# Kernel tuning notes

Hardware: AMD Instinct MI355X
Metric: run time of the kernel (lower is better)

## Reference

```python
import jax, jax.numpy as jnp
import numpy as np

N = 8192          # number of signals (rows of Y)
DIM_BASIS = 512   # signal dimension n
NUM_BASIS = 2048  # dictionary atoms m (overcomplete)
SC_ITERS = 20     # FISTA iterations
PM_ITERS = 100    # power-method iterations


def setup_inputs() -> dict:
    key = jax.random.key(0)
    kY, kW = jax.random.split(key)
    Y = jax.random.normal(kY, (N, DIM_BASIS), jnp.float32)
    W = jax.random.normal(kW, (DIM_BASIS, NUM_BASIS), jnp.float32)
    # NormDict applied in __init__: unit-norm columns
    W = W / jnp.linalg.norm(W, axis=0, keepdims=True)
    K = jnp.asarray(0.1, jnp.float32)  # lamda for FISTA soft-threshold
    return {"Y": Y, "W": W, "K": K}


def _soft(x, lam):
    return jnp.sign(x) * jax.nn.relu(jnp.abs(x) - lam)


def _power_method(W):
    # largest eigenvalue of W^T W (W: [n, m]); fixed random init for determinism
    X0 = jax.random.normal(jax.random.key(1), (1, W.shape[1]), W.dtype)

    def body(i, carry):
        X, _ = carry
        X = (X @ W.T) @ W          # X <- X W^T W, shape [1, m]
        nm = jnp.linalg.norm(X)
        return (X / nm, nm)

    _, nm = jax.lax.fori_loop(0, PM_ITERS, body, (X0, jnp.asarray(1.0, W.dtype)))
    return nm


def _fista(Y, W, lam, iters):
    c = _power_method(W)
    eta = 1.0 / c
    Gamma0 = _soft(Y @ (eta * W), lam)     # [N, m]
    Yn = jnp.linalg.norm(Y)

    def step(carry, _):
        Gamma, Z, t = carry
        residual = Z @ W.T - Y                              # [N, n]
        Gamma_new = _soft(Z - eta * (residual @ W), lam / c)
        t_new = (1.0 + jnp.sqrt(1.0 + 4.0 * t * t)) / 2.0
        Z_new = Gamma_new + ((t - 1.0) / t_new) * (Gamma_new - Gamma)
        nrm = jnp.linalg.norm(residual) / Yn
        return (Gamma_new, Z_new, t_new), nrm

    init = (Gamma0, Gamma0, jnp.asarray(1.0, Y.dtype))
    (Gamma, _, _), norms = jax.lax.scan(step, init, None, length=iters)
    return Gamma, norms


def reference(Y, W, K):
    # NormDict at start of forward (done on .data in torch -> no grad through norm)
    Wn = W / jax.lax.stop_gradient(jnp.linalg.norm(W, axis=0, keepdims=True))
    # W.requires_grad_(False) during sparse coding
    W_ng = jax.lax.stop_gradient(Wn)
    Gamma, norms = _fista(Y, W_ng, K, SC_ITERS)
    X = Gamma @ Wn.T   # reconstruction, grad flows to W here only
    return X, Gamma, norms
```

## Files before the change

### kernel.cpp

```cpp
#include <hip/hip_runtime.h>
#include <cmath>

#define NR   8192
#define DB   512
#define NB   2048
#define ITERS 20
#define NSQ   9

typedef _Float16 hfrag_t __attribute__((ext_vector_type(8)));
typedef __attribute__((ext_vector_type(4))) float accv_t;
typedef unsigned short us4 __attribute__((ext_vector_type(4)));
typedef unsigned short us8 __attribute__((ext_vector_type(8)));
typedef float f4 __attribute__((ext_vector_type(4)));

#define SL_Y2   0
#define SL_NUM  1
#define SL_DEN  2
#define SL_C    3
#define SL_ETA  4
#define SL_THR  5
#define SL_TR   6
#define SL_RES2 16

__device__ inline unsigned short f2h(float f) {
  _Float16 h = (_Float16)f;
  return __builtin_bit_cast(unsigned short, h);
}
__device__ inline float h2f(unsigned short u) {
  _Float16 h = __builtin_bit_cast(_Float16, u);
  return (float)h;
}
__device__ inline float softthr(float x, float t) {
  float a = fabsf(x) - t;
  return a > 0.f ? copysignf(a, x) : 0.f;
}


template<int MI, int NI, int NKT>
__device__ inline void gemm_tt(const unsigned short* __restrict__ At, int NTka,
                               const unsigned short* __restrict__ Bt, int NTkb,
                               int mt0, int nt0, accv_t acc[MI][NI]) {
  const int lane = threadIdx.x & 63;
  const int l16 = lane & 15, quad = lane >> 4;
  const int off = l16 * 16 + (quad & 1) * 8;
  const int kh = quad >> 1;
#pragma unroll
  for (int mi = 0; mi < MI; ++mi)
#pragma unroll
    for (int ni = 0; ni < NI; ++ni) acc[mi][ni] = (accv_t){0.f, 0.f, 0.f, 0.f};

#pragma unroll 4
  for (int kt = 0; kt < NKT; ++kt) {
    const int ktile = (kt << 1) + kh;
    hfrag_t af[MI], bf[NI];
#pragma unroll
    for (int mi = 0; mi < MI; ++mi)
      af[mi] = *(const hfrag_t*)&At[(((size_t)(mt0 + mi) * NTka + ktile) << 8) + off];
#pragma unroll
    for (int ni = 0; ni < NI; ++ni)
      bf[ni] = *(const hfrag_t*)&Bt[(((size_t)(nt0 + ni) * NTkb + ktile) << 8) + off];
#pragma unroll
    for (int mi = 0; mi < MI; ++mi)
#pragma unroll
      for (int ni = 0; ni < NI; ++ni)
        acc[mi][ni] = __builtin_amdgcn_mfma_f32_16x16x32_f16(bf[ni], af[mi], acc[mi][ni], 0, 0, 0);
  }
}

__device__ inline size_t ctile_off(int mt, int nt, int NTn) {
  int lane = threadIdx.x & 63;
  return (((size_t)mt * NTn + nt) << 8) + (lane & 15) * 16 + (lane >> 4) * 4;
}

__global__ void k_zero(float* slots, float* colsq) {
  if (threadIdx.x < 64) slots[threadIdx.x] = 0.f;
  for (int i = threadIdx.x; i < NB; i += 256) colsq[i] = 0.f;
}

__global__ void k_colsq(const float* __restrict__ W, float* __restrict__ colsq) {
  int j = blockIdx.x * 256 + threadIdx.x;
  int r0 = blockIdx.y * 64;
  float s = 0.f;
  for (int i = 0; i < 64; ++i) { float v = W[(size_t)(r0 + i) * NB + j]; s += v * v; }
  atomicAdd(&colsq[j], s);
}

__global__ void k_wnorm(const float* __restrict__ W, const float* __restrict__ colsq,
                        unsigned short* __restrict__ Wn_t, unsigned short* __restrict__ Wt_t) {
  int tx = threadIdx.x & 31, ty = threadIdx.x >> 5;
  int j = blockIdx.x * 32 + tx;
  float inv = 1.0f / sqrtf(colsq[j]);
#pragma unroll
  for (int r = 0; r < 4; ++r) {
    int i = blockIdx.y * 32 + ty + r * 8;
    unsigned short h = f2h(W[(size_t)i * NB + j] * inv);
    Wn_t[(((size_t)(i >> 4) * (NB / 16) + (j >> 4)) << 8) + (i & 15) * 16 + (j & 15)] = h;
    Wt_t[(((size_t)(j >> 4) * (DB / 16) + (i >> 4)) << 8) + (j & 15) * 16 + (i & 15)] = h;
  }
}

__global__ __launch_bounds__(256) void k_ynorm(const float* __restrict__ Y,
                                               unsigned short* __restrict__ Yh,
                                               float* __restrict__ slots) {
  __shared__ float part[4];
  int w = threadIdx.x >> 6, lane = threadIdx.x & 63;
  float s = 0.f;
#pragma unroll
  for (int rr = 0; rr < 4; ++rr) {
    int m = blockIdx.x * 16 + w * 4 + rr;
    const float* yrow = &Y[(size_t)m * DB + lane * 8];
    f4 v0 = *(const f4*)yrow;
    f4 v1 = *(const f4*)(yrow + 4);
    us8 h;
#pragma unroll
    for (int q = 0; q < 4; ++q) {
      h[q] = f2h(v0[q]);     s += v0[q] * v0[q];
      h[4 + q] = f2h(v1[q]); s += v1[q] * v1[q];
    }
    *(us8*)&Yh[(((size_t)(m >> 4) * 32 + (lane >> 1)) << 8) + (m & 15) * 16 + (lane & 1) * 8] = h;
  }
  for (int off = 32; off > 0; off >>= 1) s += __shfl_xor(s, off);
  if (lane == 0) part[w] = s;
  __syncthreads();
  if (threadIdx.x == 0) atomicAdd(&slots[SL_Y2], part[0] + part[1] + part[2] + part[3]);
}

__global__ __launch_bounds__(256) void k_sq(const float* __restrict__ S, float* __restrict__ D,
                                            const float* __restrict__ trIn, float* __restrict__ trOut) {
  __shared__ float tA[32][33], tB[32][33];
  int tx = threadIdx.x & 31, ty = threadIdx.x >> 5;
  int r0 = blockIdx.y * 32, c0 = blockIdx.x * 32;
  float inv = 1.0f / trIn[0];
  float acc[4] = {0.f, 0.f, 0.f, 0.f};
  for (int kt = 0; kt < 16; ++kt) {
    __syncthreads();
#pragma unroll
    for (int r = 0; r < 4; ++r) {
      tA[ty + r * 8][tx] = S[(size_t)(r0 + ty + r * 8) * DB + kt * 32 + tx];
      tB[ty + r * 8][tx] = S[(size_t)(kt * 32 + ty + r * 8) * DB + c0 + tx];
    }
    __syncthreads();
#pragma unroll
    for (int kk = 0; kk < 32; ++kk) {
      float b = tB[kk][tx];
#pragma unroll
      for (int r = 0; r < 4; ++r) acc[r] += tA[ty + r * 8][kk] * b;
    }
  }
  float inv2 = inv * inv;
#pragma unroll
  for (int r = 0; r < 4; ++r) {
    int row = r0 + ty + r * 8, col = c0 + tx;
    float v = acc[r] * inv2;
    D[(size_t)row * DB + col] = v;
    if (row == col) atomicAdd(trOut, v);
  }
}

__global__ void k_rayleigh(const float* __restrict__ Bm, const float* __restrict__ S,
                           float* __restrict__ slots) {
  int tid = blockIdx.x * 256 + threadIdx.x;
  float num = 0.f, den = 0.f;
  for (int i = tid; i < DB * DB; i += 256 * 256) {
    float s = S[i];
    num += Bm[i] * s;
    if ((i >> 9) == (i & 511)) den += s;
  }
  for (int off = 32; off > 0; off >>= 1) { num += __shfl_xor(num, off); den += __shfl_xor(den, off); }
  if ((threadIdx.x & 63) == 0) { atomicAdd(&slots[SL_NUM], num); atomicAdd(&slots[SL_DEN], den); }
}

__global__ void k_derive(float* slots, const float* __restrict__ Kp) {
  if (threadIdx.x == 0) {
    float cc = slots[SL_NUM] / slots[SL_DEN];
    slots[SL_C] = cc;
    float eta = 1.0f / cc;
    slots[SL_ETA] = eta;
    slots[SL_THR] = Kp[0] * eta;
  }
}

__global__ void k_norms(const float* __restrict__ slots, float* __restrict__ out) {
  int i = threadIdx.x;
  if (i < ITERS) out[i] = sqrtf(slots[SL_RES2 + i] / slots[SL_Y2]);
}

__global__ __launch_bounds__(256, 1) void k_gemm_bbuild(const unsigned short* __restrict__ Wn_t,
                                                        float* __restrict__ Bm, float* __restrict__ slots) {
  accv_t acc[2][4];
  int w = threadIdx.x >> 6, lane = threadIdx.x & 63;
  int mt0 = blockIdx.y * 8 + w * 2, nt0 = blockIdx.x * 4;
  gemm_tt<2, 4, NB / 32>(Wn_t, NB / 16, Wn_t, NB / 16, mt0, nt0, acc);
  int l16 = lane & 15, quad = lane >> 4;
  float tr = 0.f;
#pragma unroll
  for (int mi = 0; mi < 2; ++mi)
#pragma unroll
    for (int ni = 0; ni < 4; ++ni) {
      int m = (mt0 + mi) * 16 + l16, nb = (nt0 + ni) * 16 + quad * 4;
      *(f4*)&Bm[(size_t)m * DB + nb] = acc[mi][ni];
#pragma unroll
      for (int r = 0; r < 4; ++r)
        if (m == nb + r) tr += acc[mi][ni][r];
    }
  if (tr != 0.f) atomicAdd(&slots[SL_TR], tr);
}

__global__ __launch_bounds__(256) void k_gemm_init(const unsigned short* __restrict__ Yh,
                                                   const unsigned short* __restrict__ Wt_t,
                                                   const float* __restrict__ slots,
                                                   const float* __restrict__ Kp,
                                                   unsigned short* __restrict__ Gh,
                                                   unsigned short* __restrict__ Zh) {
  accv_t acc[4][4];
  int w = threadIdx.x >> 6;
  int h = blockIdx.x;
  int xcd = h & 7, slot = h >> 3;
  int band = xcd * 8 + (slot >> 4);
  int nt = slot & 15;
  int mt0 = band * 8 + (w >> 1) * 4, nt0 = nt * 8 + (w & 1) * 4;
  gemm_tt<4, 4, DB / 32>(Yh, DB / 16, Wt_t, DB / 16, mt0, nt0, acc);
  float eta = slots[SL_ETA], lam = Kp[0];
#pragma unroll
  for (int mi = 0; mi < 4; ++mi)
#pragma unroll
    for (int ni = 0; ni < 4; ++ni) {
      size_t tb = ctile_off(mt0 + mi, nt0 + ni, NB / 16);
      us4 gq;
#pragma unroll
      for (int r = 0; r < 4; ++r) gq[r] = f2h(softthr(acc[mi][ni][r] * eta, lam));
      *(us4*)&Gh[tb] = gq;
      *(us4*)&Zh[tb] = gq;
    }
}

__global__ __launch_bounds__(256, 1) void k_gemm_res(const unsigned short* __restrict__ Zh,
                                                     const unsigned short* __restrict__ Wn_t,
                                                     const unsigned short* __restrict__ Yh,
                                                     unsigned short* __restrict__ Rh,
                                                     float* __restrict__ res2slot) {
  accv_t acc[2][4];
  int w = threadIdx.x >> 6;
  int h = blockIdx.x;
  int xcd = h & 7, slot = h >> 3;
  int band = xcd * 8 + (slot >> 3);
  int nt = slot & 7;
  int mt0 = band * 8 + w * 2, nt0 = nt * 4;
  gemm_tt<2, 4, NB / 32>(Zh, NB / 16, Wn_t, NB / 16, mt0, nt0, acc);
  float s2 = 0.f;
#pragma unroll
  for (int mi = 0; mi < 2; ++mi)
#pragma unroll
    for (int ni = 0; ni < 4; ++ni) {
      size_t tb = ctile_off(mt0 + mi, nt0 + ni, DB / 16);
      us4 yq = *(const us4*)&Yh[tb];
      us4 rq;
#pragma unroll
      for (int r = 0; r < 4; ++r) {
        float rv = acc[mi][ni][r] - h2f(yq[r]);
        rq[r] = f2h(rv);
        s2 += rv * rv;
      }
      *(us4*)&Rh[tb] = rq;
    }
  for (int off = 32; off > 0; off >>= 1) s2 += __shfl_xor(s2, off);
  if ((threadIdx.x & 63) == 0) atomicAdd(res2slot, s2);
}

__global__ __launch_bounds__(256) void k_gemm_upd(const unsigned short* __restrict__ Rh,
                                                  const unsigned short* __restrict__ Wt_t,
                                                  const float* __restrict__ slots,
                                                  unsigned short* __restrict__ Gh,
                                                  unsigned short* __restrict__ Zh,
                                                  float* __restrict__ GammaOut,
                                                  float mom, int writeFinal) {
  accv_t acc[4][4];
  int w = threadIdx.x >> 6, lane = threadIdx.x & 63;
  int h = blockIdx.x;
  int xcd = h & 7, slot = h >> 3;
  int band = xcd * 8 + (slot >> 4);
  int nt = slot & 15;
  int mt0 = band * 8 + (w >> 1) * 4, nt0 = nt * 8 + (w & 1) * 4;
  gemm_tt<4, 4, DB / 32>(Rh, DB / 16, Wt_t, DB / 16, mt0, nt0, acc);
  int l16 = lane & 15, quad = lane >> 4;
  float eta = slots[SL_ETA], thr = slots[SL_THR];
#pragma unroll
  for (int mi = 0; mi < 4; ++mi)
#pragma unroll
    for (int ni = 0; ni < 4; ++ni) {
      size_t tb = ctile_off(mt0 + mi, nt0 + ni, NB / 16);
      us4 zq = *(const us4*)&Zh[tb];
      us4 gq = *(const us4*)&Gh[tb];
      us4 gho, zho;
      f4 gf;
#pragma unroll
      for (int r = 0; r < 4; ++r) {
        float z = h2f(zq[r]);
        float gold = h2f(gq[r]);
        float gn = softthr(z - eta * acc[mi][ni][r], thr);
        float zn = gn + mom * (gn - gold);
        gho[r] = f2h(gn);
        zho[r] = f2h(zn);
        gf[r] = gn;
      }
      *(us4*)&Gh[tb] = gho;
      *(us4*)&Zh[tb] = zho;
      if (writeFinal) {
        int m = (mt0 + mi) * 16 + l16, nb = (nt0 + ni) * 16 + quad * 4;
        *(f4*)&GammaOut[(size_t)m * NB + nb] = gf;
      }
    }
}

__global__ __launch_bounds__(256, 1) void k_gemm_x(const unsigned short* __restrict__ Gh,
                                                   const unsigned short* __restrict__ Wn_t,
                                                   float* __restrict__ X) {
  accv_t acc[2][4];
  int w = threadIdx.x >> 6, lane = threadIdx.x & 63;
  int h = blockIdx.x;
  int xcd = h & 7, slot = h >> 3;
  int band = xcd * 8 + (slot >> 3);
  int nt = slot & 7;
  int mt0 = band * 8 + w * 2, nt0 = nt * 4;
  gemm_tt<2, 4, NB / 32>(Gh, NB / 16, Wn_t, NB / 16, mt0, nt0, acc);
  int l16 = lane & 15, quad = lane >> 4;
#pragma unroll
  for (int mi = 0; mi < 2; ++mi)
#pragma unroll
    for (int ni = 0; ni < 4; ++ni) {
      int m = (mt0 + mi) * 16 + l16, nb = (nt0 + ni) * 16 + quad * 4;
      *(f4*)&X[(size_t)m * DB + nb] = acc[mi][ni];
    }
}

extern "C" void kernel_launch(void* const* d_in, const int* in_sizes, int n_in,
                              void* d_out, int out_size, void* d_ws, size_t ws_size,
                              hipStream_t stream) {
  const float* Y  = (const float*)d_in[0];
  const float* W  = (const float*)d_in[1];
  const float* Kp = (const float*)d_in[2];

  float* Xout     = (float*)d_out;
  float* GammaOut = Xout + (size_t)NR * DB;
  float* NormsOut = GammaOut + (size_t)NR * NB;

  char* p = (char*)d_ws;
  auto carve = [&](size_t bytes) -> void* {
    void* r = (void*)p; p += (bytes + 255) & ~(size_t)255; return r;
  };
  float* slots = (float*)carve(64 * 4);
  float* colsq = (float*)carve(NB * 4);
  float* Bmat  = (float*)carve((size_t)DB * DB * 4);
  float* S0    = (float*)carve((size_t)DB * DB * 4);
  float* S1    = (float*)carve((size_t)DB * DB * 4);
  unsigned short* Wn_t = (unsigned short*)carve((size_t)DB * NB * 2);
  unsigned short* Wt_t = (unsigned short*)carve((size_t)NB * DB * 2);
  unsigned short* Yh   = (unsigned short*)carve((size_t)NR * DB * 2);
  unsigned short* Rh   = (unsigned short*)carve((size_t)NR * DB * 2);
  unsigned short* Zh   = (unsigned short*)carve((size_t)NR * NB * 2);
  unsigned short* Gh   = (unsigned short*)carve((size_t)NR * NB * 2);

  k_zero<<<1, 256, 0, stream>>>(slots, colsq);
  k_colsq<<<dim3(NB / 256, DB / 64), 256, 0, stream>>>(W, colsq);
  k_wnorm<<<dim3(NB / 32, DB / 32), 256, 0, stream>>>(W, colsq, Wn_t, Wt_t);
  k_ynorm<<<512, 256, 0, stream>>>(Y, Yh, slots);

  k_gemm_bbuild<<<dim3(DB / 64, DB / 128), 256, 0, stream>>>(Wn_t, Bmat, slots);
  float* ss[2] = {S0, S1};
  for (int k = 0; k < NSQ; ++k) {
    const float* in = (k == 0) ? Bmat : ss[(k + 1) & 1];
    k_sq<<<dim3(16, 16), 256, 0, stream>>>(in, ss[k & 1], slots + SL_TR + k, slots + SL_TR + k + 1);
  }
  k_rayleigh<<<256, 256, 0, stream>>>(Bmat, ss[(NSQ + 1) & 1], slots);
  k_derive<<<1, 64, 0, stream>>>(slots, Kp);

  k_gemm_init<<<1024, 256, 0, stream>>>(Yh, Wt_t, slots, Kp, Gh, Zh);
  double t = 1.0;
  for (int i = 0; i < ITERS; ++i) {
    k_gemm_res<<<512, 256, 0, stream>>>(Zh, Wn_t, Yh, Rh, slots + SL_RES2 + i);
    double tn = (1.0 + sqrt(1.0 + 4.0 * t * t)) / 2.0;
    float mom = (float)((t - 1.0) / tn);
    t = tn;
    k_gemm_upd<<<1024, 256, 0, stream>>>(Rh, Wt_t, slots, Gh, Zh, GammaOut,
                                         mom, (i == ITERS - 1) ? 1 : 0);
  }
  k_gemm_x<<<512, 256, 0, stream>>>(Gh, Wn_t, Xout);
  k_norms<<<1, 64, 0, stream>>>(slots, NormsOut);
}
```

Before: 2.422 ms.

## Split K across two wave groups in residual and reconstruction GEMMs

The residual GEMM (Z·Wᵀ) and the final reconstruction GEMM now launch 512-thread blocks. Two groups of four waves each compute half of the K=2048 reduction, and the partial accumulators are summed through shared memory before the epilogue. The aim is to double the waves per output tile, which improves latency hiding and occupancy on these long-K, small-output GEMMs that previously ran only 512 blocks of 256 threads. The cost is extra LDS traffic, a block-wide barrier, an idle half-block during the epilogue, and higher LDS use per block. The launch-bounds minimum-occupancy hint is also dropped from the B-build kernel.

```diff
diff --git a/kernel.cpp b/kernel.cpp
--- a/kernel.cpp
+++ b/kernel.cpp
@@ -185,8 +185,8 @@
   if (i < ITERS) out[i] = sqrtf(slots[SL_RES2 + i] / slots[SL_Y2]);
 }
 
-__global__ __launch_bounds__(256, 1) void k_gemm_bbuild(const unsigned short* __restrict__ Wn_t,
-                                                        float* __restrict__ Bm, float* __restrict__ slots) {
+__global__ __launch_bounds__(256) void k_gemm_bbuild(const unsigned short* __restrict__ Wn_t,
+                                                     float* __restrict__ Bm, float* __restrict__ slots) {
   accv_t acc[2][4];
   int w = threadIdx.x >> 6, lane = threadIdx.x & 63;
   int mt0 = blockIdx.y * 8 + w * 2, nt0 = blockIdx.x * 4;
@@ -234,37 +234,52 @@
     }
 }
 
-__global__ __launch_bounds__(256, 1) void k_gemm_res(const unsigned short* __restrict__ Zh,
-                                                     const unsigned short* __restrict__ Wn_t,
-                                                     const unsigned short* __restrict__ Yh,
-                                                     unsigned short* __restrict__ Rh,
-                                                     float* __restrict__ res2slot) {
+__global__ __launch_bounds__(512) void k_gemm_res(const unsigned short* __restrict__ Zh,
+                                                  const unsigned short* __restrict__ Wn_t,
+                                                  const unsigned short* __restrict__ Yh,
+                                                  unsigned short* __restrict__ Rh,
+                                                  float* __restrict__ res2slot) {
+  __shared__ float red[4][64][33];
   accv_t acc[2][4];
-  int w = threadIdx.x >> 6;
+  int w = threadIdx.x >> 6, lane = threadIdx.x & 63;
+  int wk = w >> 2, wm = w & 3;
   int h = blockIdx.x;
   int xcd = h & 7, slot = h >> 3;
   int band = xcd * 8 + (slot >> 3);
   int nt = slot & 7;
-  int mt0 = band * 8 + w * 2, nt0 = nt * 4;
-  gemm_tt<2, 4, NB / 32>(Zh, NB / 16, Wn_t, NB / 16, mt0, nt0, acc);
-  float s2 = 0.f;
-#pragma unroll
-  for (int mi = 0; mi < 2; ++mi)
-#pragma unroll
-    for (int ni = 0; ni < 4; ++ni) {
-      size_t tb = ctile_off(mt0 + mi, nt0 + ni, DB / 16);
-      us4 yq = *(const us4*)&Yh[tb];
-      us4 rq;
-#pragma unroll
-      for (int r = 0; r < 4; ++r) {
-        float rv = acc[mi][ni][r] - h2f(yq[r]);
-        rq[r] = f2h(rv);
-        s2 += rv * rv;
+  int mt0 = band * 8 + wm * 2, nt0 = nt * 4;
+  const size_t koff = (size_t)wk * 64 * 256;
+  gemm_tt<2, 4, NB / 64>(Zh + koff, NB / 16, Wn_t + koff, NB / 16, mt0, nt0, acc);
+  if (wk == 1) {
+#pragma unroll
+    for (int mi = 0; mi < 2; ++mi)
+#pragma unroll
+      for (int ni = 0; ni < 4; ++ni)
+#pragma unroll
+        for (int r = 0; r < 4; ++r)
+          red[wm][lane][mi * 16 + ni * 4 + r] = acc[mi][ni][r];
+  }
+  __syncthreads();
+  if (wk == 0) {
+    float s2 = 0.f;
+#pragma unroll
+    for (int mi = 0; mi < 2; ++mi)
+#pragma unroll
+      for (int ni = 0; ni < 4; ++ni) {
+        size_t tb = ctile_off(mt0 + mi, nt0 + ni, DB / 16);
+        us4 yq = *(const us4*)&Yh[tb];
+        us4 rq;
+#pragma unroll
+        for (int r = 0; r < 4; ++r) {
+          float rv = acc[mi][ni][r] + red[wm][lane][mi * 16 + ni * 4 + r] - h2f(yq[r]);
+          rq[r] = f2h(rv);
+          s2 += rv * rv;
+        }
+        *(us4*)&Rh[tb] = rq;
       }
-      *(us4*)&Rh[tb] = rq;
-    }
-  for (int off = 32; off > 0; off >>= 1) s2 += __shfl_xor(s2, off);
-  if ((threadIdx.x & 63) == 0) atomicAdd(res2slot, s2);
+    for (int off = 32; off > 0; off >>= 1) s2 += __shfl_xor(s2, off);
+    if (lane == 0) atomicAdd(res2slot, s2);
+  }
 }
 
 __global__ __launch_bounds__(256) void k_gemm_upd(const unsigned short* __restrict__ Rh,
@@ -312,25 +327,44 @@
     }
 }
 
-__global__ __launch_bounds__(256, 1) void k_gemm_x(const unsigned short* __restrict__ Gh,
-                                                   const unsigned short* __restrict__ Wn_t,
-                                                   float* __restrict__ X) {
+__global__ __launch_bounds__(512) void k_gemm_x(const unsigned short* __restrict__ Gh,
+                                                const unsigned short* __restrict__ Wn_t,
+                                                float* __restrict__ X) {
+  __shared__ float red[4][64][33];
   accv_t acc[2][4];
   int w = threadIdx.x >> 6, lane = threadIdx.x & 63;
+  int wk = w >> 2, wm = w & 3;
   int h = blockIdx.x;
   int xcd = h & 7, slot = h >> 3;
   int band = xcd * 8 + (slot >> 3);
   int nt = slot & 7;
-  int mt0 = band * 8 + w * 2, nt0 = nt * 4;
-  gemm_tt<2, 4, NB / 32>(Gh, NB / 16, Wn_t, NB / 16, mt0, nt0, acc);
-  int l16 = lane & 15, quad = lane >> 4;
-#pragma unroll
-  for (int mi = 0; mi < 2; ++mi)
-#pragma unroll
-    for (int ni = 0; ni < 4; ++ni) {
-      int m = (mt0 + mi) * 16 + l16, nb = (nt0 + ni) * 16 + quad * 4;
-      *(f4*)&X[(size_t)m * DB + nb] = acc[mi][ni];
-    }
+  int mt0 = band * 8 + wm * 2, nt0 = nt * 4;
+  const size_t koff = (size_t)wk * 64 * 256;
+  gemm_tt<2, 4, NB / 64>(Gh + koff, NB / 16, Wn_t + koff, NB / 16, mt0, nt0, acc);
+  if (wk == 1) {
+#pragma unroll
+    for (int mi = 0; mi < 2; ++mi)
+#pragma unroll
+      for (int ni = 0; ni < 4; ++ni)
+#pragma unroll
+        for (int r = 0; r < 4; ++r)
+          red[wm][lane][mi * 16 + ni * 4 + r] = acc[mi][ni][r];
+  }
+  __syncthreads();
+  if (wk == 0) {
+    int l16 = lane & 15, quad = lane >> 4;
+#pragma unroll
+    for (int mi = 0; mi < 2; ++mi)
+#pragma unroll
+      for (int ni = 0; ni < 4; ++ni) {
+        int m = (mt0 + mi) * 16 + l16, nb = (nt0 + ni) * 16 + quad * 4;
+        f4 o;
+#pragma unroll
+        for (int r = 0; r < 4; ++r)
+          o[r] = acc[mi][ni][r] + red[wm][lane][mi * 16 + ni * 4 + r];
+        *(f4*)&X[(size_t)m * DB + nb] = o;
+      }
+  }
 }
 
 extern "C" void kernel_launch(void* const* d_in, const int* in_sizes, int n_in,
@@ -377,13 +411,13 @@
   k_gemm_init<<<1024, 256, 0, stream>>>(Yh, Wt_t, slots, Kp, Gh, Zh);
   double t = 1.0;
   for (int i = 0; i < ITERS; ++i) {
-    k_gemm_res<<<512, 256, 0, stream>>>(Zh, Wn_t, Yh, Rh, slots + SL_RES2 + i);
+    k_gemm_res<<<512, 512, 0, stream>>>(Zh, Wn_t, Yh, Rh, slots + SL_RES2 + i);
     double tn = (1.0 + sqrt(1.0 + 4.0 * t * t)) / 2.0;
     float mom = (float)((t - 1.0) / tn);
     t = tn;
     k_gemm_upd<<<1024, 256, 0, stream>>>(Rh, Wt_t, slots, Gh, Zh, GammaOut,
                                          mom, (i == ITERS - 1) ? 1 : 0);
   }
-  k_gemm_x<<<512, 256, 0, stream>>>(Gh, Wn_t, Xout);
+  k_gemm_x<<<512, 512, 0, stream>>>(Gh, Wn_t, Xout);
   k_norms<<<1, 64, 0, stream>>>(slots, NormsOut);
 }
```

Measured after the change: 2.392 ms. Within noise of the previous version (-1.2%).
